# Optimization experiments

Measured on AMD Instinct MI355X. Metric: run time of the kernel, lower is better.

## Reference

```python
import jax, jax.numpy as jnp
import numpy as np

B, S, DIN, DOUT = 4, 4096, 4096, 4096
W_SCALE = 0.02  # kaiming-ish scale; keeps values inside fp8 range


def setup_inputs() -> dict:
    key = jax.random.key(0)
    k1, k2, k3 = jax.random.split(key, 3)
    x = jax.random.normal(k1, (B, S, DIN), dtype=jnp.float16)
    weight = (jax.random.normal(k2, (DOUT, DIN), dtype=jnp.float32) * W_SCALE).astype(jnp.float16)
    bias = (jax.random.normal(k3, (DOUT,), dtype=jnp.float32) * W_SCALE).astype(jnp.float16)
    return {"x": x, "weight": weight, "bias": bias}


def reference(x, weight, bias):
    # Emulate torch._scaled_mm: activations quantized to fp8 e5m2,
    # weight (transposed) quantized to fp8 e4m3fn, scale_a = scale_b = 1.0,
    # accumulate in fp32, add fp16 bias, output fp16.
    out_shape = x.shape[:-1] + (weight.shape[0],)
    x8 = x.reshape(-1, x.shape[-1]).astype(jnp.float8_e5m2)       # [M, DIN]
    w8 = weight.T.astype(jnp.float8_e4m3fn)                        # [DIN, DOUT]
    scale = jnp.float32(1.0)  # scale_a * scale_b
    acc = jnp.matmul(x8.astype(jnp.float32), w8.astype(jnp.float32))  # [M, DOUT] fp32 accum
    out = (acc * scale + bias.astype(jnp.float32)).astype(jnp.float16)
    return out.reshape(out_shape)
```

## Files before the change

### kernel.cpp

```cpp
#include <hip/hip_runtime.h>
#include <hip/hip_fp16.h>

#define M_DIM 16384
#define N_DIM 4096
#define K_DIM 4096

typedef __attribute__((ext_vector_type(16))) float f32x16;
typedef __attribute__((ext_vector_type(4)))  int   i32x4;
typedef __attribute__((ext_vector_type(8)))  int   i32x8;

template<bool E4M3>
__global__ __launch_bounds__(256) void quant_tile_kernel(
    const float* __restrict__ in,
    uint4* __restrict__ out,
    int ngrp)
{
  int t = blockIdx.x * 256 + threadIdx.x;
  if (t >= ngrp) return;
  const int g    = t & 1023;
  const int tile = t >> 10;
  const int kt   = tile & 63;
  const int bt   = tile >> 6;
  const int sb   = g >> 7;
  const int half = (g >> 6) & 1;
  const int l    = g & 63;
  const int row  = bt * 256 + sb * 32 + (l & 31);
  const int k    = kt * 64 + (l >> 5) * 32 + half * 16;

  const float4* p = reinterpret_cast<const float4*>(in + (size_t)row * K_DIM + k);
  float4 v0 = p[0], v1 = p[1], v2 = p[2], v3 = p[3];
  int w0 = 0, w1 = 0, w2 = 0, w3 = 0;
  if (E4M3) {
    w0 = __builtin_amdgcn_cvt_pk_fp8_f32(v0.x, v0.y, w0, false);
    w0 = __builtin_amdgcn_cvt_pk_fp8_f32(v0.z, v0.w, w0, true);
    w1 = __builtin_amdgcn_cvt_pk_fp8_f32(v1.x, v1.y, w1, false);
    w1 = __builtin_amdgcn_cvt_pk_fp8_f32(v1.z, v1.w, w1, true);
    w2 = __builtin_amdgcn_cvt_pk_fp8_f32(v2.x, v2.y, w2, false);
    w2 = __builtin_amdgcn_cvt_pk_fp8_f32(v2.z, v2.w, w2, true);
    w3 = __builtin_amdgcn_cvt_pk_fp8_f32(v3.x, v3.y, w3, false);
    w3 = __builtin_amdgcn_cvt_pk_fp8_f32(v3.z, v3.w, w3, true);
  } else {
    w0 = __builtin_amdgcn_cvt_pk_bf8_f32(v0.x, v0.y, w0, false);
    w0 = __builtin_amdgcn_cvt_pk_bf8_f32(v0.z, v0.w, w0, true);
    w1 = __builtin_amdgcn_cvt_pk_bf8_f32(v1.x, v1.y, w1, false);
    w1 = __builtin_amdgcn_cvt_pk_bf8_f32(v1.z, v1.w, w1, true);
    w2 = __builtin_amdgcn_cvt_pk_bf8_f32(v2.x, v2.y, w2, false);
    w2 = __builtin_amdgcn_cvt_pk_bf8_f32(v2.z, v2.w, w2, true);
    w3 = __builtin_amdgcn_cvt_pk_bf8_f32(v3.x, v3.y, w3, false);
    w3 = __builtin_amdgcn_cvt_pk_bf8_f32(v3.z, v3.w, w3, true);
  }
  out[t] = make_uint4((unsigned)w0, (unsigned)w1, (unsigned)w2, (unsigned)w3);
}

__global__ __launch_bounds__(512, 2) void gemm_fp8_kernel(
    const unsigned char* __restrict__ Aq,
    const unsigned char* __restrict__ Wq,
    const float* __restrict__ bias,
    float* __restrict__ C)
{
  __shared__ __align__(16) unsigned char lds[65536];

  const int tid  = threadIdx.x;
  const int lane = tid & 63;
  const int wave = tid >> 6;
  const int wr   = wave >> 2;
  const int wc   = wave & 3;

  const int bid = blockIdx.x;
  const int swz = (bid & 7) * 128 + (bid >> 3);
  const int bmi = swz >> 4;
  const int bni = swz & 15;

  const unsigned char* tA = Aq + (size_t)bmi * 64 * 16384;
  const unsigned char* tB = Wq + (size_t)bni * 64 * 16384;

  const size_t t16 = (size_t)tid * 16;
  const int    w1k = wave * 1024;

#define STAGE(gbase, ldsoff)                                                \
  __builtin_amdgcn_global_load_lds(                                         \
      (const __attribute__((address_space(1))) void*)((gbase) + t16),       \
      (__attribute__((address_space(3))) void*)(lds + (ldsoff) + w1k), 16, 0, 0)

  f32x16 acc[4][2] = {};

  STAGE(tA,              0);
  STAGE(tA + 8192,       8192);
  STAGE(tB,              16384);
  STAGE(tB + 8192,       24576);
  __builtin_amdgcn_sched_barrier(0);
  STAGE(tA + 16384,          32768);
  STAGE(tA + 16384 + 8192,   40960);
  STAGE(tB + 16384,          49152);
  STAGE(tB + 16384 + 8192,   57344);
  __builtin_amdgcn_sched_barrier(0);
  asm volatile("s_waitcnt vmcnt(4)" ::: "memory");
  __builtin_amdgcn_s_barrier();

  for (int kt = 0; kt < 64; ++kt) {
    const int cur = kt & 1;
    const unsigned char* bufA = lds + cur * 32768;
    const unsigned char* bufB = bufA + 16384;
    const size_t tp2 = (size_t)((kt + 2) & 63) * 16384;

    i32x8 av0, av1, bv0, bv1;
    {
      const unsigned char* a0 = bufA + (wr * 4 + 0) * 2048 + lane * 16;
      const unsigned char* a1 = bufA + (wr * 4 + 1) * 2048 + lane * 16;
      const unsigned char* b0 = bufB + (wc * 2 + 0) * 2048 + lane * 16;
      const unsigned char* b1 = bufB + (wc * 2 + 1) * 2048 + lane * 16;
      i32x4 lo, hi;
      lo = *(const i32x4*)a0; hi = *(const i32x4*)(a0 + 1024);
      av0 = i32x8{lo.x, lo.y, lo.z, lo.w, hi.x, hi.y, hi.z, hi.w};
      lo = *(const i32x4*)a1; hi = *(const i32x4*)(a1 + 1024);
      av1 = i32x8{lo.x, lo.y, lo.z, lo.w, hi.x, hi.y, hi.z, hi.w};
      lo = *(const i32x4*)b0; hi = *(const i32x4*)(b0 + 1024);
      bv0 = i32x8{lo.x, lo.y, lo.z, lo.w, hi.x, hi.y, hi.z, hi.w};
      lo = *(const i32x4*)b1; hi = *(const i32x4*)(b1 + 1024);
      bv1 = i32x8{lo.x, lo.y, lo.z, lo.w, hi.x, hi.y, hi.z, hi.w};
    }
    __builtin_amdgcn_s_barrier();
    asm volatile("s_waitcnt lgkmcnt(0)" ::: "memory");
    __builtin_amdgcn_sched_barrier(0);
    __builtin_amdgcn_s_setprio(1);
    acc[0][0] = __builtin_amdgcn_mfma_scale_f32_32x32x64_f8f6f4(
        av0, bv0, acc[0][0], 1, 0, 0, 0x7F7F7F7F, 0, 0x7F7F7F7F);
    acc[0][1] = __builtin_amdgcn_mfma_scale_f32_32x32x64_f8f6f4(
        av0, bv1, acc[0][1], 1, 0, 0, 0x7F7F7F7F, 0, 0x7F7F7F7F);
    acc[1][0] = __builtin_amdgcn_mfma_scale_f32_32x32x64_f8f6f4(
        av1, bv0, acc[1][0], 1, 0, 0, 0x7F7F7F7F, 0, 0x7F7F7F7F);
    acc[1][1] = __builtin_amdgcn_mfma_scale_f32_32x32x64_f8f6f4(
        av1, bv1, acc[1][1], 1, 0, 0, 0x7F7F7F7F, 0, 0x7F7F7F7F);
    __builtin_amdgcn_s_setprio(0);
    __builtin_amdgcn_s_barrier();
    __builtin_amdgcn_sched_barrier(0);

    STAGE(tB + tp2,        cur * 32768 + 16384);
    STAGE(tB + tp2 + 8192, cur * 32768 + 24576);
    i32x8 av2, av3;
    {
      const unsigned char* a2 = bufA + (wr * 4 + 2) * 2048 + lane * 16;
      const unsigned char* a3 = bufA + (wr * 4 + 3) * 2048 + lane * 16;
      i32x4 lo, hi;
      lo = *(const i32x4*)a2; hi = *(const i32x4*)(a2 + 1024);
      av2 = i32x8{lo.x, lo.y, lo.z, lo.w, hi.x, hi.y, hi.z, hi.w};
      lo = *(const i32x4*)a3; hi = *(const i32x4*)(a3 + 1024);
      av3 = i32x8{lo.x, lo.y, lo.z, lo.w, hi.x, hi.y, hi.z, hi.w};
    }
    __builtin_amdgcn_s_barrier();
    asm volatile("s_waitcnt lgkmcnt(0)" ::: "memory");
    __builtin_amdgcn_sched_barrier(0);
    __builtin_amdgcn_s_setprio(1);
    acc[2][0] = __builtin_amdgcn_mfma_scale_f32_32x32x64_f8f6f4(
        av2, bv0, acc[2][0], 1, 0, 0, 0x7F7F7F7F, 0, 0x7F7F7F7F);
    acc[2][1] = __builtin_amdgcn_mfma_scale_f32_32x32x64_f8f6f4(
        av2, bv1, acc[2][1], 1, 0, 0, 0x7F7F7F7F, 0, 0x7F7F7F7F);
    acc[3][0] = __builtin_amdgcn_mfma_scale_f32_32x32x64_f8f6f4(
        av3, bv0, acc[3][0], 1, 0, 0, 0x7F7F7F7F, 0, 0x7F7F7F7F);
    acc[3][1] = __builtin_amdgcn_mfma_scale_f32_32x32x64_f8f6f4(
        av3, bv1, acc[3][1], 1, 0, 0, 0x7F7F7F7F, 0, 0x7F7F7F7F);
    __builtin_amdgcn_s_setprio(0);
    __builtin_amdgcn_s_barrier();
    __builtin_amdgcn_sched_barrier(0);

    STAGE(tA + tp2,        cur * 32768);
    STAGE(tA + tp2 + 8192, cur * 32768 + 8192);
    asm volatile("s_waitcnt vmcnt(4)" ::: "memory");
    __builtin_amdgcn_s_barrier();
  }
#undef STAGE

  #pragma unroll
  for (int n = 0; n < 2; ++n) {
    const int col = bni * 256 + wc * 64 + n * 32 + (lane & 31);
    const float bv = bias[col];
    #pragma unroll
    for (int m = 0; m < 4; ++m) {
      const int rbase = bmi * 256 + wr * 128 + m * 32 + ((lane >> 5) << 2);
      #pragma unroll
      for (int r = 0; r < 16; ++r) {
        const int row = rbase + (r & 3) + 8 * (r >> 2);
        C[(size_t)row * N_DIM + col] =
            __half2float(__float2half_rn(acc[m][n][r] + bv));
      }
    }
  }
}

extern "C" void kernel_launch(void* const* d_in, const int* in_sizes, int n_in,
                              void* d_out, int out_size, void* d_ws, size_t ws_size,
                              hipStream_t stream) {
  const float* x  = (const float*)d_in[0];
  const float* w  = (const float*)d_in[1];
  const float* bs = (const float*)d_in[2];
  float* out = (float*)d_out;

  unsigned char* xq = (unsigned char*)d_ws;
  unsigned char* wq = (unsigned char*)d_ws + (size_t)M_DIM * K_DIM;

  const int ngx = (M_DIM * K_DIM) / 16;
  const int ngw = (N_DIM * K_DIM) / 16;
  quant_tile_kernel<false><<<ngx / 256, 256, 0, stream>>>(x, (uint4*)xq, ngx);
  quant_tile_kernel<true ><<<ngw / 256, 256, 0, stream>>>(w, (uint4*)wq, ngw);

  gemm_fp8_kernel<<<1024, 512, 0, stream>>>(xq, wq, bs, out);
}
```

Baseline: 356.6 us.

## Software-pipeline LDS fragment reads against MFMAs with register double-buffering

```diff
diff --git a/kernel.cpp b/kernel.cpp
--- a/kernel.cpp
+++ b/kernel.cpp
@@ -82,7 +82,22 @@
       (const __attribute__((address_space(1))) void*)((gbase) + t16),       \
       (__attribute__((address_space(3))) void*)(lds + (ldsoff) + w1k), 16, 0, 0)
 
+#define RDFRAG(dst, byteoff)                                                \
+  { const unsigned char* _p = lds + (byteoff) + lane * 16;                  \
+    i32x4 _lo = *(const i32x4*)_p;                                          \
+    i32x4 _hi = *(const i32x4*)(_p + 1024);                                 \
+    dst = i32x8{_lo.x, _lo.y, _lo.z, _lo.w, _hi.x, _hi.y, _hi.z, _hi.w}; }
+
+#define MFMA(d, a, b)                                                       \
+  d = __builtin_amdgcn_mfma_scale_f32_32x32x64_f8f6f4(                      \
+      a, b, d, 1 , 0 , 0, 0x7F7F7F7F, 0, 0x7F7F7F7F)
+
+  const int aoff = wr * 8192;
+  const int boff = 16384 + wc * 4096;
+
   f32x16 acc[4][2] = {};
+  i32x8 aE0, aE1, aE2, aE3, bE0, bE1;
+  i32x8 aO0, aO1, aO2, aO3, bO0, bO1;
 
   STAGE(tA,              0);
   STAGE(tA + 8192,       8192);
@@ -96,79 +111,68 @@
   __builtin_amdgcn_sched_barrier(0);
   asm volatile("s_waitcnt vmcnt(4)" ::: "memory");
   __builtin_amdgcn_s_barrier();
-
-  for (int kt = 0; kt < 64; ++kt) {
-    const int cur = kt & 1;
-    const unsigned char* bufA = lds + cur * 32768;
-    const unsigned char* bufB = bufA + 16384;
-    const size_t tp2 = (size_t)((kt + 2) & 63) * 16384;
-
-    i32x8 av0, av1, bv0, bv1;
+  RDFRAG(aE0, aoff + 0 * 2048);  RDFRAG(aE1, aoff + 1 * 2048);
+  RDFRAG(aE2, aoff + 2 * 2048);  RDFRAG(aE3, aoff + 3 * 2048);
+  RDFRAG(bE0, boff + 0 * 2048);  RDFRAG(bE1, boff + 1 * 2048);
+  asm volatile("s_waitcnt lgkmcnt(0)" ::: "memory");
+  __builtin_amdgcn_sched_barrier(0);
+  __builtin_amdgcn_s_barrier();
+
+  for (int kt = 0; kt < 64; kt += 2) {
     {
-      const unsigned char* a0 = bufA + (wr * 4 + 0) * 2048 + lane * 16;
-      const unsigned char* a1 = bufA + (wr * 4 + 1) * 2048 + lane * 16;
-      const unsigned char* b0 = bufB + (wc * 2 + 0) * 2048 + lane * 16;
-      const unsigned char* b1 = bufB + (wc * 2 + 1) * 2048 + lane * 16;
-      i32x4 lo, hi;
-      lo = *(const i32x4*)a0; hi = *(const i32x4*)(a0 + 1024);
-      av0 = i32x8{lo.x, lo.y, lo.z, lo.w, hi.x, hi.y, hi.z, hi.w};
-      lo = *(const i32x4*)a1; hi = *(const i32x4*)(a1 + 1024);
-      av1 = i32x8{lo.x, lo.y, lo.z, lo.w, hi.x, hi.y, hi.z, hi.w};
-      lo = *(const i32x4*)b0; hi = *(const i32x4*)(b0 + 1024);
-      bv0 = i32x8{lo.x, lo.y, lo.z, lo.w, hi.x, hi.y, hi.z, hi.w};
-      lo = *(const i32x4*)b1; hi = *(const i32x4*)(b1 + 1024);
-      bv1 = i32x8{lo.x, lo.y, lo.z, lo.w, hi.x, hi.y, hi.z, hi.w};
+      const size_t tp = (size_t)((kt + 2) & 63) * 16384;
+      STAGE(tA + tp,        0);
+      STAGE(tA + tp + 8192, 8192);
+      STAGE(tB + tp,        16384);
+      STAGE(tB + tp + 8192, 24576);
+      asm volatile("s_waitcnt vmcnt(4)" ::: "memory");
+      __builtin_amdgcn_s_barrier();
+      RDFRAG(aO0, 32768 + aoff + 0 * 2048);
+      RDFRAG(aO1, 32768 + aoff + 1 * 2048);
+      RDFRAG(aO2, 32768 + aoff + 2 * 2048);
+      RDFRAG(aO3, 32768 + aoff + 3 * 2048);
+      RDFRAG(bO0, 32768 + boff + 0 * 2048);
+      RDFRAG(bO1, 32768 + boff + 1 * 2048);
+      __builtin_amdgcn_s_setprio(1);
+      MFMA(acc[0][0], aE0, bE0); MFMA(acc[0][1], aE0, bE1);
+      MFMA(acc[1][0], aE1, bE0); MFMA(acc[1][1], aE1, bE1);
+      MFMA(acc[2][0], aE2, bE0); MFMA(acc[2][1], aE2, bE1);
+      MFMA(acc[3][0], aE3, bE0); MFMA(acc[3][1], aE3, bE1);
+      __builtin_amdgcn_s_setprio(0);
+      __builtin_amdgcn_sched_barrier(0);
+      asm volatile("s_waitcnt lgkmcnt(0)" ::: "memory");
+      __builtin_amdgcn_sched_barrier(0);
+      __builtin_amdgcn_s_barrier();
     }
-    __builtin_amdgcn_s_barrier();
-    asm volatile("s_waitcnt lgkmcnt(0)" ::: "memory");
-    __builtin_amdgcn_sched_barrier(0);
-    __builtin_amdgcn_s_setprio(1);
-    acc[0][0] = __builtin_amdgcn_mfma_scale_f32_32x32x64_f8f6f4(
-        av0, bv0, acc[0][0], 1, 0, 0, 0x7F7F7F7F, 0, 0x7F7F7F7F);
-    acc[0][1] = __builtin_amdgcn_mfma_scale_f32_32x32x64_f8f6f4(
-        av0, bv1, acc[0][1], 1, 0, 0, 0x7F7F7F7F, 0, 0x7F7F7F7F);
-    acc[1][0] = __builtin_amdgcn_mfma_scale_f32_32x32x64_f8f6f4(
-        av1, bv0, acc[1][0], 1, 0, 0, 0x7F7F7F7F, 0, 0x7F7F7F7F);
-    acc[1][1] = __builtin_amdgcn_mfma_scale_f32_32x32x64_f8f6f4(
-        av1, bv1, acc[1][1], 1, 0, 0, 0x7F7F7F7F, 0, 0x7F7F7F7F);
-    __builtin_amdgcn_s_setprio(0);
-    __builtin_amdgcn_s_barrier();
-    __builtin_amdgcn_sched_barrier(0);
-
-    STAGE(tB + tp2,        cur * 32768 + 16384);
-    STAGE(tB + tp2 + 8192, cur * 32768 + 24576);
-    i32x8 av2, av3;
     {
-      const unsigned char* a2 = bufA + (wr * 4 + 2) * 2048 + lane * 16;
-      const unsigned char* a3 = bufA + (wr * 4 + 3) * 2048 + lane * 16;
-      i32x4 lo, hi;
-      lo = *(const i32x4*)a2; hi = *(const i32x4*)(a2 + 1024);
-      av2 = i32x8{lo.x, lo.y, lo.z, lo.w, hi.x, hi.y, hi.z, hi.w};
-      lo = *(const i32x4*)a3; hi = *(const i32x4*)(a3 + 1024);
-      av3 = i32x8{lo.x, lo.y, lo.z, lo.w, hi.x, hi.y, hi.z, hi.w};
+      const size_t tp = (size_t)((kt + 3) & 63) * 16384;
+      STAGE(tA + tp,        32768);
+      STAGE(tA + tp + 8192, 40960);
+      STAGE(tB + tp,        49152);
+      STAGE(tB + tp + 8192, 57344);
+      asm volatile("s_waitcnt vmcnt(4)" ::: "memory");
+      __builtin_amdgcn_s_barrier();
+      RDFRAG(aE0, aoff + 0 * 2048);
+      RDFRAG(aE1, aoff + 1 * 2048);
+      RDFRAG(aE2, aoff + 2 * 2048);
+      RDFRAG(aE3, aoff + 3 * 2048);
+      RDFRAG(bE0, boff + 0 * 2048);
+      RDFRAG(bE1, boff + 1 * 2048);
+      __builtin_amdgcn_s_setprio(1);
+      MFMA(acc[0][0], aO0, bO0); MFMA(acc[0][1], aO0, bO1);
+      MFMA(acc[1][0], aO1, bO0); MFMA(acc[1][1], aO1, bO1);
+      MFMA(acc[2][0], aO2, bO0); MFMA(acc[2][1], aO2, bO1);
+      MFMA(acc[3][0], aO3, bO0); MFMA(acc[3][1], aO3, bO1);
+      __builtin_amdgcn_s_setprio(0);
+      __builtin_amdgcn_sched_barrier(0);
+      asm volatile("s_waitcnt lgkmcnt(0)" ::: "memory");
+      __builtin_amdgcn_sched_barrier(0);
+      __builtin_amdgcn_s_barrier();
     }
-    __builtin_amdgcn_s_barrier();
-    asm volatile("s_waitcnt lgkmcnt(0)" ::: "memory");
-    __builtin_amdgcn_sched_barrier(0);
-    __builtin_amdgcn_s_setprio(1);
-    acc[2][0] = __builtin_amdgcn_mfma_scale_f32_32x32x64_f8f6f4(
-        av2, bv0, acc[2][0], 1, 0, 0, 0x7F7F7F7F, 0, 0x7F7F7F7F);
-    acc[2][1] = __builtin_amdgcn_mfma_scale_f32_32x32x64_f8f6f4(
-        av2, bv1, acc[2][1], 1, 0, 0, 0x7F7F7F7F, 0, 0x7F7F7F7F);
-    acc[3][0] = __builtin_amdgcn_mfma_scale_f32_32x32x64_f8f6f4(
-        av3, bv0, acc[3][0], 1, 0, 0, 0x7F7F7F7F, 0, 0x7F7F7F7F);
-    acc[3][1] = __builtin_amdgcn_mfma_scale_f32_32x32x64_f8f6f4(
-        av3, bv1, acc[3][1], 1, 0, 0, 0x7F7F7F7F, 0, 0x7F7F7F7F);
-    __builtin_amdgcn_s_setprio(0);
-    __builtin_amdgcn_s_barrier();
-    __builtin_amdgcn_sched_barrier(0);
-
-    STAGE(tA + tp2,        cur * 32768);
-    STAGE(tA + tp2 + 8192, cur * 32768 + 8192);
-    asm volatile("s_waitcnt vmcnt(4)" ::: "memory");
-    __builtin_amdgcn_s_barrier();
   }
 #undef STAGE
+#undef RDFRAG
+#undef MFMA
 
   #pragma unroll
   for (int n = 0; n < 2; ++n) {
```

New measurement: 358.2 us. No clear change (+0.4%).
